# Kernel optimization log

Hardware: AMD Instinct MI355X
Metric: run time of the kernel (lower is better)

## Reference

```python
import jax, jax.numpy as jnp
from jax import lax
import numpy as np

NUM_CENTROIDS = 1024
RADIUS = 0.5
K = 32
EPS = 1e-5


def _fps(xyz, num_samples):
    """Farthest point sampling. Deterministic start at index 0 (torch uses randint)."""
    B, N, _ = xyz.shape

    def step(carry, _):
        distances, farthest = carry
        centroid = jnp.take_along_axis(xyz, farthest[:, None, None], axis=1)  # [B,1,3]
        d = jnp.sum((xyz - centroid) ** 2, axis=-1)  # [B,N]
        distances = jnp.minimum(distances, d)
        nxt = jnp.argmax(distances, axis=-1).astype(jnp.int32)
        return (distances, nxt), farthest

    init = (jnp.full((B, N), jnp.inf, dtype=xyz.dtype), jnp.zeros((B,), jnp.int32))
    _, idxs = lax.scan(step, init, None, length=num_samples)  # [M,B]
    return jnp.transpose(idxs)  # [B,M]


def _ball_query(xyz, new_xyz):
    """K nearest neighbors within RADIUS; out-of-ball slots fall back to nearest."""
    d2 = (jnp.sum(new_xyz ** 2, -1)[:, :, None] + jnp.sum(xyz ** 2, -1)[:, None, :]
          - 2.0 * jnp.einsum('bmd,bnd->bmn', new_xyz, xyz))
    dist = jnp.sqrt(jnp.maximum(d2, 0.0))  # [B,M,N] cdist
    dist = jnp.where(dist > RADIUS, jnp.inf, dist)
    neg_vals, idx = lax.top_k(-dist, K)  # smallest-K distances
    mask = jnp.isinf(neg_vals)  # outside radius
    idx = jnp.where(mask, idx[:, :, 0:1], idx)
    return idx  # [B,M,K]


def _forward(xyz, features, Ws, bs, gs, bts):
    B, N, _ = xyz.shape
    cidx = lax.stop_gradient(_fps(xyz, NUM_CENTROIDS))  # [B,M] int
    new_xyz = jnp.take_along_axis(xyz, cidx[:, :, None], axis=1)  # [B,M,3]
    gidx = lax.stop_gradient(_ball_query(xyz, new_xyz))  # [B,M,K] int
    flat = gidx.reshape(B, -1)
    gxyz = jnp.take_along_axis(xyz, flat[:, :, None], axis=1).reshape(B, NUM_CENTROIDS, K, 3)
    gxyz = gxyz - new_xyz[:, :, None, :]
    gfeat = jnp.take_along_axis(features, flat[:, :, None], axis=1).reshape(B, NUM_CENTROIDS, K, -1)
    h = jnp.concatenate([gxyz, gfeat], axis=-1)  # [B,M,K,C+3]
    for W, b, g, bt in zip(Ws, bs, gs, bts):
        # 1x1 Conv1d == per-point linear over channels
        h = jnp.einsum('bmkc,oc->bmko', h, W) + b
        # BatchNorm1d in training mode: batch stats over (B*M, K), biased var
        mu = jnp.mean(h, axis=(0, 1, 2))
        var = jnp.var(h, axis=(0, 1, 2))
        h = (h - mu) * lax.rsqrt(var + EPS) * g + bt
        h = jax.nn.gelu(h, approximate=False)  # torch nn.GELU default (exact erf)
    return new_xyz, jnp.max(h, axis=2)  # [B,M,3], [B,M,128]


def setup_inputs() -> dict:
    key = jax.random.key(0)
    ks = jax.random.split(key, 8)
    B, N, C = 8, 8192, 64
    xyz = jax.random.normal(ks[0], (B, N, 3), jnp.float32)
    features = jax.random.normal(ks[1], (B, N, C), jnp.float32)
    chans = [C + 3, 64, 64, 128]
    inp = {"xyz": xyz, "features": features}
    for l in range(3):
        cin, cout = chans[l], chans[l + 1]
        inp[f"W{l + 1}"] = jax.random.normal(ks[2 + l], (cout, cin), jnp.float32) / jnp.float32(np.sqrt(cin))
        inp[f"b{l + 1}"] = jnp.zeros((cout,), jnp.float32)
        inp[f"g{l + 1}"] = jnp.ones((cout,), jnp.float32)
        inp[f"bt{l + 1}"] = jnp.zeros((cout,), jnp.float32)
    return inp


def reference(xyz, features, W1, b1, g1, bt1, W2, b2, g2, bt2, W3, b3, g3, bt3):
    return _forward(xyz, features, (W1, W2, W3), (b1, b2, b3), (g1, g2, g3), (bt1, bt2, bt3))
```

## Files before the change

### kernel.cpp

```cpp
#include <hip/hip_runtime.h>
#include <cstdint>
#include <cstddef>

#define BATCH 8
#define NPTS  8192
#define MCENT 1024
#define KNN   32
#define CFEAT 64
#define EPS_F 1e-5f

#define WS_NEED 73400320ull

__device__ __forceinline__ float erf_fast(float x) {
  float a = fabsf(x);
  float t = __builtin_amdgcn_rcpf(fmaf(0.3275911f, a, 1.0f));
  float p = fmaf(1.061405429f, t, -1.453152027f);
  p = fmaf(p, t, 1.421413741f);
  p = fmaf(p, t, -0.284496736f);
  p = fmaf(p, t, 0.254829592f);
  float e = __expf(-a * a);
  float y = fmaf(-p * t, e, 1.0f);
  return copysignf(y, x);
}
__device__ __forceinline__ float gelu_f(float x) {
  return 0.5f * x * (1.0f + erf_fast(x * 0.70710678118654752440f));
}

template<int CTRL>
__device__ __forceinline__ float dpp_max_step(float v) {
  int s = __builtin_amdgcn_update_dpp(__float_as_int(v), __float_as_int(v),
                                      CTRL, 0xf, 0xf, false);
  return fmaxf(v, __int_as_float(s));
}
__device__ __forceinline__ float wave_max_dpp(float v) {
  v = dpp_max_step<0x111>(v);
  v = dpp_max_step<0x112>(v);
  v = dpp_max_step<0x114>(v);
  v = dpp_max_step<0x118>(v);
  v = dpp_max_step<0x142>(v);
  v = dpp_max_step<0x143>(v);
  return v;
}
template<int CTRL>
__device__ __forceinline__ unsigned long long dpp_min64_step(unsigned long long v) {
  int lo = __builtin_amdgcn_update_dpp((int)(unsigned)(v & 0xffffffffull),
                                       (int)(unsigned)(v & 0xffffffffull),
                                       CTRL, 0xf, 0xf, false);
  int hi = __builtin_amdgcn_update_dpp((int)(unsigned)(v >> 32),
                                       (int)(unsigned)(v >> 32),
                                       CTRL, 0xf, 0xf, false);
  unsigned long long o = (((unsigned long long)(unsigned)hi) << 32) | (unsigned)lo;
  return o < v ? o : v;
}
__device__ __forceinline__ unsigned long long wave_min64_dpp(unsigned long long v) {
  v = dpp_min64_step<0x111>(v);
  v = dpp_min64_step<0x112>(v);
  v = dpp_min64_step<0x114>(v);
  v = dpp_min64_step<0x118>(v);
  v = dpp_min64_step<0x142>(v);
  v = dpp_min64_step<0x143>(v);
  return v;
}

template<int M, int HALF>
__device__ __forceinline__ void tree_step(float* s_, float* q_, int lane) {
  bool up = (lane & M) != 0;
#pragma unroll
  for (int j = 0; j < HALF; ++j) {
    float ks = up ? s_[j+HALF] : s_[j];
    float ds = up ? s_[j]      : s_[j+HALF];
    s_[j] = ks + __shfl_xor(ds, M, 64);
    float kq = up ? q_[j+HALF] : q_[j];
    float dq = up ? q_[j]      : q_[j+HALF];
    q_[j] = kq + __shfl_xor(dq, M, 64);
  }
}
template<int M, int HALF>
__device__ __forceinline__ void ptree_step(float* g_, int kbit) {
  bool up = (kbit & M) != 0;
#pragma unroll
  for (int j = 0; j < HALF; ++j) {
    float kv = up ? g_[j+HALF] : g_[j];
    float dv = up ? g_[j]      : g_[j+HALF];
    g_[j] = fmaxf(kv, __shfl_xor(dv, M, 64));
  }
}

#define FPS_STEPS 64
#define BQCAP 512
__global__ __launch_bounds__(512, 1) void mega_kernel(
    const float* __restrict__ xyz, float* __restrict__ new_xyz,
    float* __restrict__ dist_ws, float* __restrict__ cst, int s0,
    int* __restrict__ gidx, const float* __restrict__ feats,
    const float* __restrict__ W1, const float* __restrict__ b1v,
    float* __restrict__ h1)
{
  __shared__ float pts[NPTS * 3];
  __shared__ float outb[FPS_STEPS * 3];
  __shared__ unsigned long long keys[2][8];
  __shared__ unsigned long long list[8][BQCAP];
  int blk = blockIdx.x, t = threadIdx.x;

  if (blk < 8) {
    if (s0 >= MCENT) return;
    int b = blk;
    const float* xb = xyz + (size_t)b * NPTS * 3;
    float px[16], py[16], pz[16], dist[16];
    {
      const float4* src = (const float4*)(xb + (size_t)t * 48);
      float4 buf[12];
#pragma unroll
      for (int i = 0; i < 12; ++i) buf[i] = src[i];
      const float* f = (const float*)buf;
#pragma unroll
      for (int i = 0; i < 16; ++i) {
        px[i] = f[i*3+0]; py[i] = f[i*3+1]; pz[i] = f[i*3+2];
      }
      float4* dst = (float4*)(pts + (size_t)t * 48);
#pragma unroll
      for (int i = 0; i < 12; ++i) dst[i] = buf[i];
    }
    float* dw = dist_ws + (size_t)b * NPTS + (size_t)t * 16;
    float cx, cy, cz;
    if (s0 == 0) {
#pragma unroll
      for (int i = 0; i < 16; ++i) dist[i] = __builtin_inff();
      cx = xb[0]; cy = xb[1]; cz = xb[2];
    } else {
      float4 d0 = *(const float4*)(dw + 0);
      float4 d1 = *(const float4*)(dw + 4);
      float4 d2 = *(const float4*)(dw + 8);
      float4 d3 = *(const float4*)(dw + 12);
      dist[0]=d0.x; dist[1]=d0.y; dist[2]=d0.z; dist[3]=d0.w;
      dist[4]=d1.x; dist[5]=d1.y; dist[6]=d1.z; dist[7]=d1.w;
      dist[8]=d2.x; dist[9]=d2.y; dist[10]=d2.z; dist[11]=d2.w;
      dist[12]=d3.x; dist[13]=d3.y; dist[14]=d3.z; dist[15]=d3.w;
      cx = cst[b*3+0]; cy = cst[b*3+1]; cz = cst[b*3+2];
    }
    int lane = t & 63, wv = t >> 6;

    for (int s = 0; s < FPS_STEPS; ++s) {
      if (t == 0) { outb[s*3+0] = cx; outb[s*3+1] = cy; outb[s*3+2] = cz; }
      float bd = -1.0f; int bslot = 0;
#pragma unroll
      for (int i = 0; i < 16; ++i) {
        float dx = __fsub_rn(px[i], cx);
        float dy = __fsub_rn(py[i], cy);
        float dz = __fsub_rn(pz[i], cz);
        float d  = __fadd_rn(__fadd_rn(__fmul_rn(dx,dx), __fmul_rn(dy,dy)), __fmul_rn(dz,dz));
        float nd = fminf(dist[i], d);
        dist[i] = nd;
        if (nd > bd) { bd = nd; bslot = i; }
      }
      float w = wave_max_dpp(bd);
      float wmax = __int_as_float(__builtin_amdgcn_readlane(__float_as_int(w), 63));
      unsigned long long mk = __ballot(bd == wmax);
      int sl = __ffsll((long long)mk) - 1;
      int widx = __builtin_amdgcn_readlane(t * 16 + bslot, sl);
      if (lane == 0)
        keys[s & 1][wv] = (((unsigned long long)__float_as_uint(wmax)) << 32)
                          | (unsigned)(8191 - widx);
      __syncthreads();
      unsigned long long bk = keys[s & 1][0];
#pragma unroll
      for (int w2 = 1; w2 < 8; ++w2) {
        unsigned long long o = keys[s & 1][w2];
        if (o > bk) bk = o;
      }
      int idx = 8191 - (int)(unsigned)(bk & 0xffffffffull);
      cx = pts[idx*3+0]; cy = pts[idx*3+1]; cz = pts[idx*3+2];
    }

    *(float4*)(dw + 0)  = make_float4(dist[0], dist[1], dist[2], dist[3]);
    *(float4*)(dw + 4)  = make_float4(dist[4], dist[5], dist[6], dist[7]);
    *(float4*)(dw + 8)  = make_float4(dist[8], dist[9], dist[10], dist[11]);
    *(float4*)(dw + 12) = make_float4(dist[12], dist[13], dist[14], dist[15]);
    if (t == 0) { cst[b*3+0] = cx; cst[b*3+1] = cy; cst[b*3+2] = cz; }
    __syncthreads();
    float* ob = new_xyz + (size_t)b * MCENT * 3 + (size_t)s0 * 3;
    for (int i = t; i < FPS_STEPS * 3; i += 512) ob[i] = outb[i];

  } else if (blk < 72) {
    int ph = s0 - FPS_STEPS;
    if (ph < 0 || ph >= MCENT) return;
    int wv = t >> 6, lane = t & 63;
    int c  = (blk - 8) * 8 + wv;
    int b  = c >> 6;
    int ci = ph + (c & 63);
    int gm = b * MCENT + ci;
    const float* cc = new_xyz + (size_t)gm * 3;
    float c0 = cc[0], c1 = cc[1], c2 = cc[2];
    float sc = __fadd_rn(__fadd_rn(__fmul_rn(c0,c0), __fmul_rn(c1,c1)), __fmul_rn(c2,c2));
    const float* xb = xyz + (size_t)b * NPTS * 3;

    unsigned cnt = 0;
    for (int j0 = 0; j0 < NPTS; j0 += 64) {
      int j = j0 + lane;
      float x = xb[j*3+0], y = xb[j*3+1], z = xb[j*3+2];
      float sx  = __fadd_rn(__fadd_rn(__fmul_rn(x,x), __fmul_rn(y,y)), __fmul_rn(z,z));
      float dot = __fadd_rn(__fadd_rn(__fmul_rn(c0,x), __fmul_rn(c1,y)), __fmul_rn(c2,z));
      float d2  = __fsub_rn(__fadd_rn(sc, sx), __fmul_rn(2.0f, dot));
      float dist = sqrtf(fmaxf(d2, 0.0f));
      bool in_ = (dist <= 0.5f);
      unsigned long long mask = __ballot(in_);
      unsigned off = (unsigned)__popcll(mask & ((1ull << lane) - 1ull));
      if (in_) {
        unsigned pos = cnt + off;
        if (pos < BQCAP)
          list[wv][pos] = (((unsigned long long)__float_as_uint(dist)) << 32) | (unsigned)j;
      }
      cnt += (unsigned)__popcll(mask);
    }
    if (cnt > BQCAP) cnt = BQCAP;

    unsigned long long e[8];
#pragma unroll
    for (int i = 0; i < 8; ++i) {
      unsigned pos = (unsigned)lane + ((unsigned)i << 6);
      e[i] = (pos < cnt) ? list[wv][pos] : ~0ull;
    }
#define CE_(a_, b_) { bool sw = e[b_] < e[a_]; \
                      unsigned long long lo_ = sw ? e[b_] : e[a_]; \
                      unsigned long long hi_ = sw ? e[a_] : e[b_]; \
                      e[a_] = lo_; e[b_] = hi_; }
    CE_(0,1) CE_(2,3) CE_(4,5) CE_(6,7)
    CE_(0,2) CE_(1,3) CE_(4,6) CE_(5,7)
    CE_(1,2) CE_(5,6)
    CE_(0,4) CE_(1,5) CE_(2,6) CE_(3,7)
    CE_(2,4) CE_(3,5)
    CE_(1,2) CE_(3,4) CE_(5,6)
#undef CE_

    int* gout = gidx + (size_t)gm * KNN;
    int first = 0;
    int kmax = (cnt < (unsigned)KNN) ? (int)cnt : KNN;
    for (int k = 0; k < KNN; ++k) {
      if (k < kmax) {
        unsigned long long wr = wave_min64_dpp(e[0]);
        unsigned lo32 = (unsigned)__builtin_amdgcn_readlane((int)(unsigned)(wr & 0xffffffffull), 63);
        unsigned hi32 = (unsigned)__builtin_amdgcn_readlane((int)(unsigned)(wr >> 32), 63);
        unsigned long long wmin = (((unsigned long long)hi32) << 32) | lo32;
        int idxv = (int)lo32;
        if (k == 0) first = idxv;
        if (lane == 0) gout[k] = idxv;
        bool win = (e[0] == wmin);
#pragma unroll
        for (int i = 0; i < 7; ++i) e[i] = win ? e[i+1] : e[i];
        e[7] = win ? ~0ull : e[7];
      } else {
        if (lane == 0) gout[k] = first;
      }
    }

  } else if (blk < 104) {
    int ph = s0 - 2 * FPS_STEPS;
    if (ph < 0) return;
    int row = (blk - 72) * 512 + t;
    int c   = row >> 5;
    int k   = row & 31;
    int b   = c >> 6;
    int ci  = ph + (c & 63);
    int p   = b * (MCENT * KNN) + ci * KNN + k;
    int idx = gidx[p];
    const float* cc = new_xyz + (size_t)(b * MCENT + ci) * 3;
    const float* q  = xyz + (size_t)(b * NPTS + idx) * 3;
    float in[67];
    in[0] = q[0] - cc[0];
    in[1] = q[1] - cc[1];
    in[2] = q[2] - cc[2];
    const float* fr = feats + (size_t)(b * NPTS + idx) * CFEAT;
#pragma unroll
    for (int j = 0; j < 64; j += 4) {
      float4 v = *(const float4*)(fr + j);
      in[3+j] = v.x; in[4+j] = v.y; in[5+j] = v.z; in[6+j] = v.w;
    }
    float* orow = h1 + (size_t)p * 64;
    for (int o4 = 0; o4 < 16; ++o4) {
      const float* w0 = W1 + (size_t)(o4 * 4) * 67;
      float a0 = b1v[o4*4+0], a1 = b1v[o4*4+1], a2 = b1v[o4*4+2], a3 = b1v[o4*4+3];
#pragma unroll
      for (int j = 0; j < 67; ++j) {
        float x = in[j];
        a0 = fmaf(x, w0[j],       a0);
        a1 = fmaf(x, w0[67+j],    a1);
        a2 = fmaf(x, w0[134+j],   a2);
        a3 = fmaf(x, w0[201+j],   a3);
      }
      *(float4*)(orow + o4*4) = make_float4(a0, a1, a2, a3);
    }
  }
}

__global__ __launch_bounds__(256) void l2_kernel(
    float* __restrict__ h, const float* __restrict__ W,
    const float* __restrict__ bv, const float* __restrict__ bnp,
    const float* __restrict__ btp)
{
  int p = blockIdx.x * 256 + threadIdx.x;
  float* row = h + (size_t)p * 64;
  float in[64];
#pragma unroll
  for (int j = 0; j < 64; j += 4) {
    float4 v = *(const float4*)(row + j);
    in[j+0] = gelu_f((v.x - bnp[j+0]) * bnp[64+j+0] + btp[j+0]);
    in[j+1] = gelu_f((v.y - bnp[j+1]) * bnp[64+j+1] + btp[j+1]);
    in[j+2] = gelu_f((v.z - bnp[j+2]) * bnp[64+j+2] + btp[j+2]);
    in[j+3] = gelu_f((v.w - bnp[j+3]) * bnp[64+j+3] + btp[j+3]);
  }
  for (int o4 = 0; o4 < 16; ++o4) {
    const float* w0 = W + (size_t)(o4 * 4) * 64;
    float a0 = bv[o4*4+0], a1 = bv[o4*4+1], a2 = bv[o4*4+2], a3 = bv[o4*4+3];
#pragma unroll
    for (int j = 0; j < 64; ++j) {
      float x = in[j];
      a0 = fmaf(x, w0[j],      a0);
      a1 = fmaf(x, w0[64+j],   a1);
      a2 = fmaf(x, w0[128+j],  a2);
      a3 = fmaf(x, w0[192+j],  a3);
    }
    *(float4*)(row + o4*4) = make_float4(a0, a1, a2, a3);
  }
}

template<int C>
__global__ __launch_bounds__(256) void stats_kernel(const float* __restrict__ h,
                                                    float* __restrict__ part)
{
  constexpr int G = 256 / C;
  int t = threadIdx.x;
  int c = t % C, g = t / C;
  const float* base = h + (size_t)blockIdx.x * 512 * C;
  float s = 0.0f, ss = 0.0f;
  for (int r = g; r < 512; r += G) {
    float v = base[(size_t)r * C + c];
    s += v;
    ss = fmaf(v, v, ss);
  }
  __shared__ float ls[256], lss[256];
  ls[t] = s; lss[t] = ss;
  __syncthreads();
  if (g == 0) {
    for (int gg = 1; gg < G; ++gg) { s += ls[gg*C + c]; ss += lss[gg*C + c]; }
    part[(size_t)blockIdx.x * (2*C) + c]     = s;
    part[(size_t)blockIdx.x * (2*C) + C + c] = ss;
  }
}

template<int C>
__global__ __launch_bounds__(256) void fin_kernel(const float* __restrict__ part,
                                                  const float* __restrict__ gv,
                                                  float* __restrict__ bn)
{
  int c = blockIdx.x, t = threadIdx.x;
  float s = 0.0f, ss = 0.0f;
  for (int b2 = t; b2 < 512; b2 += 256) {
    s  += part[(size_t)b2 * (2*C) + c];
    ss += part[(size_t)b2 * (2*C) + C + c];
  }
  __shared__ float ls[256], lss[256];
  ls[t] = s; lss[t] = ss;
  __syncthreads();
  for (int k = 128; k > 0; k >>= 1) {
    if (t < k) { ls[t] += ls[t+k]; lss[t] += lss[t+k]; }
    __syncthreads();
  }
  if (t == 0) {
    const float inv_n = 1.0f / 262144.0f;
    float mu  = ls[0] * inv_n;
    float var = fmaxf(lss[0] * inv_n - mu * mu, 0.0f);
    bn[c]     = mu;
    bn[C + c] = gv[c] / sqrtf(var + EPS_F);
  }
}

__global__ __launch_bounds__(256) void act_kernel(float* __restrict__ h,
                                                  const float* __restrict__ bnp,
                                                  const float* __restrict__ btp)
{
  int p = blockIdx.x * 256 + threadIdx.x;
  float* row = h + (size_t)p * 64;
#pragma unroll
  for (int j = 0; j < 64; j += 4) {
    float4 v = *(const float4*)(row + j);
    v.x = gelu_f((v.x - bnp[j+0]) * bnp[64+j+0] + btp[j+0]);
    v.y = gelu_f((v.y - bnp[j+1]) * bnp[64+j+1] + btp[j+1]);
    v.z = gelu_f((v.z - bnp[j+2]) * bnp[64+j+2] + btp[j+2]);
    v.w = gelu_f((v.w - bnp[j+3]) * bnp[64+j+3] + btp[j+3]);
    *(float4*)(row + j) = v;
  }
}

__global__ __launch_bounds__(256, 1) void l3stats_kernel(
    const float* __restrict__ g2, const float* __restrict__ W3,
    const float* __restrict__ b3, float* __restrict__ part)
{
  int t = threadIdx.x;
  int gb = blockIdx.x >> 2, chunk = blockIdx.x & 3;
  int og0 = chunk * 32;
  int p = gb * 256 + t;
  const float* row = g2 + (size_t)p * 64;
  float in[64];
#pragma unroll
  for (int j = 0; j < 64; j += 4) {
    float4 v = *(const float4*)(row + j);
    in[j+0] = v.x; in[j+1] = v.y; in[j+2] = v.z; in[j+3] = v.w;
  }
  float s_[32], q_[32];
  for (int o4 = 0; o4 < 8; ++o4) {
    const float* w0 = W3 + (size_t)(og0 + o4 * 4) * 64;
    float a0 = b3[og0+o4*4+0], a1 = b3[og0+o4*4+1], a2 = b3[og0+o4*4+2], a3 = b3[og0+o4*4+3];
#pragma unroll
    for (int j = 0; j < 64; ++j) {
      float x = in[j];
      a0 = fmaf(x, w0[j],      a0);
      a1 = fmaf(x, w0[64+j],   a1);
      a2 = fmaf(x, w0[128+j],  a2);
      a3 = fmaf(x, w0[192+j],  a3);
    }
    int o = o4 * 4;
    s_[o]=a0; s_[o+1]=a1; s_[o+2]=a2; s_[o+3]=a3;
    q_[o]=a0*a0; q_[o+1]=a1*a1; q_[o+2]=a2*a2; q_[o+3]=a3*a3;
  }

  int wv = t >> 6, lane = t & 63;
  tree_step<1,16>(s_, q_, lane);
  tree_step<2, 8>(s_, q_, lane);
  tree_step<4, 4>(s_, q_, lane);
  tree_step<8, 2>(s_, q_, lane);
  tree_step<16,1>(s_, q_, lane);
  s_[0] += __shfl_xor(s_[0], 32, 64);
  q_[0] += __shfl_xor(q_[0], 32, 64);

  int ch = (int)(__brev((unsigned)(lane & 31)) >> 27);
  float* pw = part + ((size_t)blockIdx.x * 4 + wv) * 64;
  if (lane < 32) { pw[ch] = s_[0]; pw[32 + ch] = q_[0]; }
}

__global__ __launch_bounds__(256) void fin3_kernel(const float* __restrict__ part,
                                                   const float* __restrict__ gv,
                                                   float* __restrict__ bn)
{
  int c = blockIdx.x, t = threadIdx.x;
  int chunk = c >> 5, j = c & 31;
  float s = 0.0f, ss = 0.0f;
  for (int gb = t; gb < 1024; gb += 256) {
    int blk = gb * 4 + chunk;
#pragma unroll
    for (int wv = 0; wv < 4; ++wv) {
      const float* pw = part + ((size_t)blk * 4 + wv) * 64;
      s  += pw[j];
      ss += pw[32 + j];
    }
  }
  __shared__ float ls[256], lss[256];
  ls[t] = s; lss[t] = ss;
  __syncthreads();
  for (int k = 128; k > 0; k >>= 1) {
    if (t < k) { ls[t] += ls[t+k]; lss[t] += lss[t+k]; }
    __syncthreads();
  }
  if (t == 0) {
    const float inv_n = 1.0f / 262144.0f;
    float mu  = ls[0] * inv_n;
    float var = fmaxf(lss[0] * inv_n - mu * mu, 0.0f);
    bn[c]       = mu;
    bn[128 + c] = gv[c] / sqrtf(var + EPS_F);
  }
}

__global__ __launch_bounds__(256, 1) void pool3_kernel(
    const float* __restrict__ g2, const float* __restrict__ W3,
    const float* __restrict__ b3,
    const float* __restrict__ bnp3,
    const float* __restrict__ btp3,
    float* __restrict__ out1)
{
  int t = threadIdx.x;
  int gb = blockIdx.x >> 1, og0 = (blockIdx.x & 1) * 64;
  int p = gb * 256 + t;
  const float* row = g2 + (size_t)p * 64;
  float in[64];
#pragma unroll
  for (int j = 0; j < 64; j += 4) {
    float4 v = *(const float4*)(row + j);
    in[j+0] = v.x; in[j+1] = v.y; in[j+2] = v.z; in[j+3] = v.w;
  }
  float g_[64];
  for (int o4 = 0; o4 < 16; ++o4) {
    const float* w0 = W3 + (size_t)(og0 + o4 * 4) * 64;
    float a0 = b3[og0+o4*4+0], a1 = b3[og0+o4*4+1], a2 = b3[og0+o4*4+2], a3 = b3[og0+o4*4+3];
#pragma unroll
    for (int j = 0; j < 64; ++j) {
      float x = in[j];
      a0 = fmaf(x, w0[j],      a0);
      a1 = fmaf(x, w0[64+j],   a1);
      a2 = fmaf(x, w0[128+j],  a2);
      a3 = fmaf(x, w0[192+j],  a3);
    }
    int oc0 = og0 + o4 * 4, o = o4 * 4;
    g_[o]   = gelu_f((a0 - bnp3[oc0+0]) * bnp3[128+oc0+0] + btp3[oc0+0]);
    g_[o+1] = gelu_f((a1 - bnp3[oc0+1]) * bnp3[128+oc0+1] + btp3[oc0+1]);
    g_[o+2] = gelu_f((a2 - bnp3[oc0+2]) * bnp3[128+oc0+2] + btp3[oc0+2]);
    g_[o+3] = gelu_f((a3 - bnp3[oc0+3]) * bnp3[128+oc0+3] + btp3[oc0+3]);
  }

  ptree_step<1,32>(g_, t);
  ptree_step<2,16>(g_, t);
  ptree_step<4, 8>(g_, t);
  ptree_step<8, 4>(g_, t);
  ptree_step<16,2>(g_, t);

  int ch0 = (int)(__brev((unsigned)(t & 31)) >> 27) * 2;
  int gm = gb * 8 + (t >> 5);
  out1[(size_t)gm * 128 + og0 + ch0]     = g_[0];
  out1[(size_t)gm * 128 + og0 + ch0 + 1] = g_[1];
}

__global__ void fill_kernel(float* __restrict__ out1) {
  out1[blockIdx.x * 256 + threadIdx.x] = 1.0e6f;
}

extern "C" void kernel_launch(void* const* d_in, const int* in_sizes, int n_in,
                              void* d_out, int out_size, void* d_ws, size_t ws_size,
                              hipStream_t stream)
{
  (void)in_sizes; (void)n_in; (void)out_size;
  const float* xyz   = (const float*)d_in[0];
  const float* feats = (const float*)d_in[1];
  const float* W1  = (const float*)d_in[2];
  const float* b1  = (const float*)d_in[3];
  const float* g1  = (const float*)d_in[4];
  const float* bt1 = (const float*)d_in[5];
  const float* W2  = (const float*)d_in[6];
  const float* b2  = (const float*)d_in[7];
  const float* g2  = (const float*)d_in[8];
  const float* bt2 = (const float*)d_in[9];
  const float* W3  = (const float*)d_in[10];
  const float* b3  = (const float*)d_in[11];
  const float* g3  = (const float*)d_in[12];
  const float* bt3 = (const float*)d_in[13];

  float* out0 = (float*)d_out;
  float* out1 = out0 + (size_t)BATCH * MCENT * 3;

  char* ws = (char*)d_ws;
  int*   gidx    = (int*)(ws + 0);
  float* part    = (float*)(ws + (1u << 20));
  float* bn0     = (float*)(ws + 5u * (1u << 20));
  float* bn1     = bn0 + 128;
  float* bn2     = bn0 + 256;
  float* dist_ws = (float*)(ws + 5u * (1u << 20) + 65536u);
  float* cst     = (float*)(ws + 5u * (1u << 20) + 65536u + 262144u);
  float* h1      = (float*)(ws + 6u * (1u << 20));

  if (ws_size < WS_NEED) {
    fill_kernel<<<4096, 256, 0, stream>>>(out1);
    return;
  }

  for (int s0 = 0; s0 <= MCENT + FPS_STEPS; s0 += FPS_STEPS)
    mega_kernel<<<104, 512, 0, stream>>>(xyz, out0, dist_ws, cst, s0,
                                         gidx, feats, W1, b1, h1);

  stats_kernel<64><<<512, 256, 0, stream>>>(h1, part);
  fin_kernel<64><<<64, 256, 0, stream>>>(part, g1, bn0);
  l2_kernel<<<1024, 256, 0, stream>>>(h1, W2, b2, bn0, bt1);
  stats_kernel<64><<<512, 256, 0, stream>>>(h1, part);
  fin_kernel<64><<<64, 256, 0, stream>>>(part, g2, bn1);
  act_kernel<<<1024, 256, 0, stream>>>(h1, bn1, bt2);
  l3stats_kernel<<<4096, 256, 0, stream>>>(h1, W3, b3, part);
  fin3_kernel<<<128, 256, 0, stream>>>(part, g3, bn2);
  pool3_kernel<<<2048, 256, 0, stream>>>(h1, W3, b3, bn2, bt3, out1);
}
```

Before: 1.554 ms.

## Fold layer-1 BN stats into pipelined mega kernel; split pool3 into four channel chunks

Adds a third stage of blocks to the pipelined mega kernel. These blocks compute per-channel sum and sum-of-squares of h1 one step behind the layer-1 conv blocks, and the standalone stats kernel launch is removed. The mega-kernel loop gets one extra iteration to drain the new stage. Separately, pool3 now processes 32 output channels per block over four times as many blocks, which lowers register pressure but recomputes the input load more often. The partial-sum layout must match what fin_kernel expects; the shared arrays add LDS to a kernel that already uses a lot of it.

```diff
diff --git a/kernel.cpp b/kernel.cpp
--- a/kernel.cpp
+++ b/kernel.cpp
@@ -93,12 +93,13 @@
     float* __restrict__ dist_ws, float* __restrict__ cst, int s0,
     int* __restrict__ gidx, const float* __restrict__ feats,
     const float* __restrict__ W1, const float* __restrict__ b1v,
-    float* __restrict__ h1)
+    float* __restrict__ h1, float* __restrict__ part)
 {
   __shared__ float pts[NPTS * 3];
   __shared__ float outb[FPS_STEPS * 3];
   __shared__ unsigned long long keys[2][8];
   __shared__ unsigned long long list[8][BQCAP];
+  __shared__ float ls[512], lss[512];
   int blk = blockIdx.x, t = threadIdx.x;
 
   if (blk < 8) {
@@ -254,7 +255,7 @@
 
   } else if (blk < 104) {
     int ph = s0 - 2 * FPS_STEPS;
-    if (ph < 0) return;
+    if (ph < 0 || ph >= MCENT) return;
     int row = (blk - 72) * 512 + t;
     int c   = row >> 5;
     int k   = row & 31;
@@ -288,6 +289,30 @@
       }
       *(float4*)(orow + o4*4) = make_float4(a0, a1, a2, a3);
     }
+
+  } else {
+    int ph = s0 - 3 * FPS_STEPS;
+    if (ph < 0 || ph >= MCENT) return;
+    int sb = blk - 104;
+    int b  = sb >> 2;
+    int rb = (sb & 3) * 512;
+    int c  = t & 63, g = t >> 6;
+    size_t base = (size_t)b * (MCENT * KNN) + (size_t)ph * KNN + rb;
+    float s = 0.0f, ss = 0.0f;
+    for (int r = g; r < 512; r += 8) {
+      float v = h1[(base + r) * 64 + c];
+      s += v;
+      ss = fmaf(v, v, ss);
+    }
+    ls[t] = s; lss[t] = ss;
+    __syncthreads();
+    if (g == 0) {
+#pragma unroll
+      for (int gg = 1; gg < 8; ++gg) { s += ls[gg*64 + c]; ss += lss[gg*64 + c]; }
+      int pblk = (ph >> 6) * 32 + sb;
+      part[(size_t)pblk * 128 + c]      = s;
+      part[(size_t)pblk * 128 + 64 + c] = ss;
+    }
   }
 }
 
@@ -476,7 +501,8 @@
     float* __restrict__ out1)
 {
   int t = threadIdx.x;
-  int gb = blockIdx.x >> 1, og0 = (blockIdx.x & 1) * 64;
+  int gb = blockIdx.x >> 2, chunk = blockIdx.x & 3;
+  int og0 = chunk * 32;
   int p = gb * 256 + t;
   const float* row = g2 + (size_t)p * 64;
   float in[64];
@@ -485,8 +511,8 @@
     float4 v = *(const float4*)(row + j);
     in[j+0] = v.x; in[j+1] = v.y; in[j+2] = v.z; in[j+3] = v.w;
   }
-  float g_[64];
-  for (int o4 = 0; o4 < 16; ++o4) {
+  float g_[32];
+  for (int o4 = 0; o4 < 8; ++o4) {
     const float* w0 = W3 + (size_t)(og0 + o4 * 4) * 64;
     float a0 = b3[og0+o4*4+0], a1 = b3[og0+o4*4+1], a2 = b3[og0+o4*4+2], a3 = b3[og0+o4*4+3];
 #pragma unroll
@@ -504,16 +530,15 @@
     g_[o+3] = gelu_f((a3 - bnp3[oc0+3]) * bnp3[128+oc0+3] + btp3[oc0+3]);
   }
 
-  ptree_step<1,32>(g_, t);
-  ptree_step<2,16>(g_, t);
-  ptree_step<4, 8>(g_, t);
-  ptree_step<8, 4>(g_, t);
-  ptree_step<16,2>(g_, t);
-
-  int ch0 = (int)(__brev((unsigned)(t & 31)) >> 27) * 2;
+  ptree_step<1,16>(g_, t);
+  ptree_step<2, 8>(g_, t);
+  ptree_step<4, 4>(g_, t);
+  ptree_step<8, 2>(g_, t);
+  ptree_step<16,1>(g_, t);
+
+  int ch = (int)(__brev((unsigned)(t & 31)) >> 27);
   int gm = gb * 8 + (t >> 5);
-  out1[(size_t)gm * 128 + og0 + ch0]     = g_[0];
-  out1[(size_t)gm * 128 + og0 + ch0 + 1] = g_[1];
+  out1[(size_t)gm * 128 + og0 + ch] = g_[0];
 }
 
 __global__ void fill_kernel(float* __restrict__ out1) {
@@ -558,11 +583,10 @@
     return;
   }
 
-  for (int s0 = 0; s0 <= MCENT + FPS_STEPS; s0 += FPS_STEPS)
-    mega_kernel<<<104, 512, 0, stream>>>(xyz, out0, dist_ws, cst, s0,
-                                         gidx, feats, W1, b1, h1);
-
-  stats_kernel<64><<<512, 256, 0, stream>>>(h1, part);
+  for (int s0 = 0; s0 <= MCENT + 2 * FPS_STEPS; s0 += FPS_STEPS)
+    mega_kernel<<<136, 512, 0, stream>>>(xyz, out0, dist_ws, cst, s0,
+                                         gidx, feats, W1, b1, h1, part);
+
   fin_kernel<64><<<64, 256, 0, stream>>>(part, g1, bn0);
   l2_kernel<<<1024, 256, 0, stream>>>(h1, W2, b2, bn0, bt1);
   stats_kernel<64><<<512, 256, 0, stream>>>(h1, part);
@@ -570,5 +594,5 @@
   act_kernel<<<1024, 256, 0, stream>>>(h1, bn1, bt2);
   l3stats_kernel<<<4096, 256, 0, stream>>>(h1, W3, b3, part);
   fin3_kernel<<<128, 256, 0, stream>>>(part, g3, bn2);
-  pool3_kernel<<<2048, 256, 0, stream>>>(h1, W3, b3, bn2, bt3, out1);
-}
+  pool3_kernel<<<4096, 256, 0, stream>>>(h1, W3, b3, bn2, bt3, out1);
+}
```

Result: faster. 1.500 ms (-3.5%).
